# Optimization experiments

Hardware: AMD Instinct MI355X
Metric: run time of the kernel (lower is better)

The kernel has to match this reference:

```python
import jax, jax.numpy as jnp
import numpy as np

N, E, F_IN, H, C, L = 100000, 1600000, 128, 64, 16, 3
NEG_SLOPE_ATT = 0.2   # GATConv attention leaky_relu
NEG_SLOPE_ACT = 0.01  # F.leaky_relu default


def setup_inputs() -> dict:
    key = jax.random.key(0)
    ks = jax.random.split(key, 12)
    x = jax.random.normal(ks[0], (N, F_IN), dtype=jnp.float32)
    edge_index = jax.random.randint(ks[1], (2, E), 0, N, dtype=jnp.int64)
    edge_weight = jax.random.uniform(ks[2], (E,), dtype=jnp.float32)
    s = 0.05
    W_in = jax.random.normal(ks[3], (F_IN, H), dtype=jnp.float32) * s
    b_in = jnp.zeros((H,), dtype=jnp.float32)
    Wc = jax.random.normal(ks[4], (L, H, H), dtype=jnp.float32) * s
    a_src = jax.random.normal(ks[5], (L, H), dtype=jnp.float32) * s
    a_dst = jax.random.normal(ks[6], (L, H), dtype=jnp.float32) * s
    bc = jnp.zeros((L, H), dtype=jnp.float32)
    W_out = jax.random.normal(ks[7], (H, C), dtype=jnp.float32) * s
    b_out = jnp.zeros((C,), dtype=jnp.float32)
    return {"x": x, "edge_index": edge_index, "edge_weight": edge_weight,
            "W_in": W_in, "b_in": b_in, "Wc": Wc, "a_src": a_src,
            "a_dst": a_dst, "bc": bc, "W_out": W_out, "b_out": b_out}


def _gat_layer(h, src, dst, W, asrc, adst, b):
    # linear transform (no bias on lin in PyG GATConv)
    h = h @ W                                   # [N, H]
    # per-node attention contributions
    alpha_s = h @ asrc                          # [N]
    alpha_d = h @ adst                          # [N]
    e = jax.nn.leaky_relu(alpha_s[src] + alpha_d[dst], NEG_SLOPE_ATT)  # [E']
    # segment softmax over destination nodes
    m = jax.ops.segment_max(e, dst, num_segments=N)
    ex = jnp.exp(e - m[dst])
    denom = jax.ops.segment_sum(ex, dst, num_segments=N)
    w = ex / (denom[dst] + 1e-16)
    # weighted scatter-add aggregation
    out = jax.ops.segment_sum(h[src] * w[:, None], dst, num_segments=N)
    return out + b


def reference(x, edge_index, edge_weight, W_in, b_in, Wc, a_src, a_dst, bc, W_out, b_out):
    # add self-loops (PyG GATConv default)
    loops = jnp.arange(N, dtype=edge_index.dtype)
    src = jnp.concatenate([edge_index[0], loops])
    dst = jnp.concatenate([edge_index[1], loops])

    h = jax.nn.leaky_relu(x @ W_in + b_in, NEG_SLOPE_ACT)
    for l in range(L):
        h = jax.nn.leaky_relu(_gat_layer(h, src, dst, Wc[l], a_src[l], a_dst[l], bc[l]), NEG_SLOPE_ACT)
    logits = h @ W_out + b_out
    return jax.nn.log_softmax(logits, axis=-1)
```

## Files before the change

### kernel.cpp

```cpp
#include <hip/hip_runtime.h>

#define N_NODES 100000
#define E_EDGES 1600000
#define F_IN    128
#define H_DIM   64
#define C_OUT   16
#define L_LAYERS 3
#define NTOT    (E_EDGES + N_NODES)
#define MAXD    64

#define BKN2    512
#define NB2     ((N_NODES + BKN2 - 1) / BKN2)
#define BCAP    9216
#define CH      8192
#define PB      ((E_EDGES + CH - 1) / CH)

__device__ inline unsigned short f2bf(float f) {
    unsigned u = __float_as_uint(f);
    return (unsigned short)((u + 0x7FFFu + ((u >> 16) & 1u)) >> 16);
}
__device__ inline float bf_lo(unsigned p) { return __uint_as_float(p << 16); }
__device__ inline float bf_hi(unsigned p) { return __uint_as_float(p & 0xFFFF0000u); }

__global__ void detect64_kernel(const unsigned int* __restrict__ e, int* flag) {
    __shared__ int s_any;
    if (threadIdx.x == 0) s_any = 0;
    __syncthreads();
    int any = 0;
    for (int i = threadIdx.x; i < 2048; i += 256)
        if (e[2 * i + 1] != 0u) any = 1;
    if (any) atomicOr(&s_any, 1);
    __syncthreads();
    if (threadIdx.x == 0) *flag = s_any ? 0 : 1;
}

__global__ __launch_bounds__(256) void bucket_scatter2(
        const void* __restrict__ eidx, const int* __restrict__ flag,
        int* __restrict__ bcur, unsigned int* __restrict__ packed) {
    __shared__ int cnt[NB2], basel[NB2], curl[NB2], gbase[NB2];
    __shared__ int sd[256];
    __shared__ unsigned int stage[CH];
    __shared__ unsigned char bkt[CH];
    int t = threadIdx.x;
    int b0 = blockIdx.x * CH;
    int ne = min(CH, E_EDGES - b0);
    for (int i = t; i < NB2; i += 256) cnt[i] = 0;
    __syncthreads();

    int f64 = *flag;
    int es[CH / 256], ed[CH / 256];
    #pragma unroll
    for (int j = 0; j < CH / 256; ++j) {
        int idx = b0 + j * 256 + t;
        if (idx < E_EDGES) {
            if (f64) {
                es[j] = (int)((const long long*)eidx)[idx];
                ed[j] = (int)((const long long*)eidx)[E_EDGES + idx];
            } else {
                es[j] = ((const int*)eidx)[idx];
                ed[j] = ((const int*)eidx)[E_EDGES + idx];
            }
            atomicAdd(&cnt[ed[j] >> 9], 1);
        } else { es[j] = -1; }
    }
    __syncthreads();
    int v = (t < NB2) ? cnt[t] : 0;
    sd[t] = v;
    __syncthreads();
    for (int off = 1; off < 256; off <<= 1) {
        int u = (t >= off) ? sd[t - off] : 0;
        __syncthreads();
        sd[t] += u;
        __syncthreads();
    }
    if (t < NB2) {
        basel[t] = sd[t] - v;
        curl[t] = 0;
        gbase[t] = atomicAdd(&bcur[t], v);
    }
    __syncthreads();
    #pragma unroll
    for (int j = 0; j < CH / 256; ++j) {
        if (es[j] >= 0) {
            int b = ed[j] >> 9;
            int r = atomicAdd(&curl[b], 1);
            int pos = basel[b] + r;
            stage[pos] = ((unsigned)(ed[j] & (BKN2 - 1)) << 17) | (unsigned)es[j];
            bkt[pos] = (unsigned char)b;
        }
    }
    __syncthreads();
    for (int i = t; i < ne; i += 256) {
        int b = bkt[i];
        packed[(size_t)b * BCAP + gbase[b] + (i - basel[b])] = stage[i];
    }
}

__global__ __launch_bounds__(256) void bucket_scan2(
        const int* __restrict__ bcur, int* __restrict__ ebase) {
    __shared__ int sd[256];
    int t = threadIdx.x;
    int v = (t < NB2) ? bcur[t] : 0;
    sd[t] = v;
    __syncthreads();
    for (int off = 1; off < 256; off <<= 1) {
        int u = (t >= off) ? sd[t - off] : 0;
        __syncthreads();
        sd[t] += u;
        __syncthreads();
    }
    if (t < NB2) ebase[t] = sd[t] - v;
}

__global__ __launch_bounds__(256) void csr_build2(
        const unsigned int* __restrict__ packed, const int* __restrict__ bcur,
        const int* __restrict__ ebase,
        int* __restrict__ row_ptr, int* __restrict__ csr_src) {
    __shared__ int cnt[BKN2], scn[BKN2], cur[BKN2];
    int b = blockIdx.x, t = threadIdx.x;
    int nbase = b * BKN2;
    int nn = min(BKN2, N_NODES - nbase);
    int ec = bcur[b];
    size_t pbase = (size_t)b * BCAP;
    int cbase = ebase[b] + nbase;
    cnt[t] = (t < nn) ? 1 : 0;
    cnt[t + 256] = (t + 256 < nn) ? 1 : 0;
    __syncthreads();
    for (int i = t; i < ec; i += 256)
        atomicAdd(&cnt[packed[pbase + i] >> 17], 1);
    __syncthreads();
    scn[t] = cnt[t];
    scn[t + 256] = cnt[t + 256];
    __syncthreads();
    for (int off = 1; off < BKN2; off <<= 1) {
        int u0 = (t >= off) ? scn[t - off] : 0;
        int u1 = (t + 256 >= off) ? scn[t + 256 - off] : 0;
        __syncthreads();
        scn[t] += u0;
        scn[t + 256] += u1;
        __syncthreads();
    }
    #pragma unroll
    for (int q = 0; q < 2; ++q) {
        int idx = t + q * 256;
        if (idx < nn) {
            int offi = scn[idx] - cnt[idx];
            row_ptr[nbase + idx] = cbase + offi;
            csr_src[cbase + offi] = nbase + idx;
            cur[idx] = offi + 1;
        }
    }
    if (b == NB2 - 1 && t == 0) row_ptr[N_NODES] = cbase + ec + nn;
    __syncthreads();
    for (int i = t; i < ec; i += 256) {
        unsigned p = packed[pbase + i];
        int dl = p >> 17, s = (int)(p & 0x1FFFFu);
        int pos = atomicAdd(&cur[dl], 1);
        csr_src[cbase + pos] = s;
    }
}

#define GBR 64
#define KC  64
#define SAP (KC + 4)

template<int K, bool ACT, bool DOTS, bool ABF16>
__global__ __launch_bounds__(256) void gemm_lds_kernel(
        const void* __restrict__ Ain, const float* __restrict__ W,
        const float* __restrict__ bias,
        const float* __restrict__ asrc, const float* __restrict__ adst,
        unsigned* __restrict__ C, float* __restrict__ as_, float* __restrict__ ad_) {
    __shared__ __align__(16) float sW[KC * 64];
    __shared__ __align__(16) float sA[GBR][SAP];
    int t = threadIdx.x;
    int r0 = blockIdx.x * GBR;
    int wave = t >> 6, lane = t & 63;
    int tr = wave * 4 + (lane >> 4);
    int c0 = (lane & 15) * 4;

    float acc[4][4];
    #pragma unroll
    for (int i = 0; i < 4; ++i)
        #pragma unroll
        for (int j = 0; j < 4; ++j) acc[i][j] = 0.f;

    for (int kc = 0; kc < K; kc += KC) {
        if (kc) __syncthreads();
        {
            const float4* W4 = (const float4*)(W + kc * 64);
            float4* sW4 = (float4*)sW;
            for (int i = t; i < KC * 16; i += 256) sW4[i] = W4[i];
        }
        if (ABF16) {
            const unsigned* A32 = (const unsigned*)Ain;
            for (int it = 0; it < (GBR * KC / 4) / 256; ++it) {
                int idx = it * 256 + t;
                int r = idx >> 4;
                int c2 = idx & 15;
                int gr = r0 + r;
                uint2 pv = make_uint2(0u, 0u);
                if (gr < N_NODES)
                    pv = *(const uint2*)&A32[(size_t)gr * (K / 2) + kc / 2 + c2 * 2];
                sA[r][c2 * 4 + 0] = bf_lo(pv.x);
                sA[r][c2 * 4 + 1] = bf_hi(pv.x);
                sA[r][c2 * 4 + 2] = bf_lo(pv.y);
                sA[r][c2 * 4 + 3] = bf_hi(pv.y);
            }
        } else {
            const float* A = (const float*)Ain;
            for (int it = 0; it < (GBR * KC / 4) / 256; ++it) {
                int idx = it * 256 + t;
                int r = idx >> 4;
                int c4 = idx & 15;
                int gr = r0 + r;
                float4 v = make_float4(0.f, 0.f, 0.f, 0.f);
                if (gr < N_NODES) v = *(const float4*)&A[(size_t)gr * K + kc + c4 * 4];
                *(float4*)&sA[r][c4 * 4] = v;
            }
        }
        __syncthreads();
        #pragma unroll 2
        for (int kk = 0; kk < KC; kk += 4) {
            float4 w0 = *(const float4*)&sW[(kk + 0) * 64 + c0];
            float4 w1 = *(const float4*)&sW[(kk + 1) * 64 + c0];
            float4 w2 = *(const float4*)&sW[(kk + 2) * 64 + c0];
            float4 w3 = *(const float4*)&sW[(kk + 3) * 64 + c0];
            #pragma unroll
            for (int i = 0; i < 4; ++i) {
                float4 a = *(const float4*)&sA[tr + 16 * i][kk];
                acc[i][0] += a.x * w0.x + a.y * w1.x + a.z * w2.x + a.w * w3.x;
                acc[i][1] += a.x * w0.y + a.y * w1.y + a.z * w2.y + a.w * w3.y;
                acc[i][2] += a.x * w0.z + a.y * w1.z + a.z * w2.z + a.w * w3.z;
                acc[i][3] += a.x * w0.w + a.y * w1.w + a.z * w2.w + a.w * w3.w;
            }
        }
    }

    float bs[4] = {0.f, 0.f, 0.f, 0.f};
    float av[4], dv[4];
    if (ACT) {
        #pragma unroll
        for (int j = 0; j < 4; ++j) bs[j] = bias[c0 + j];
    }
    if (DOTS) {
        #pragma unroll
        for (int j = 0; j < 4; ++j) { av[j] = asrc[c0 + j]; dv[j] = adst[c0 + j]; }
    }
    #pragma unroll
    for (int i = 0; i < 4; ++i) {
        int grow = r0 + tr + 16 * i;
        if (grow >= N_NODES) continue;
        float v0 = acc[i][0], v1 = acc[i][1], v2 = acc[i][2], v3 = acc[i][3];
        if (ACT) {
            v0 += bs[0]; v0 = v0 > 0.f ? v0 : 0.01f * v0;
            v1 += bs[1]; v1 = v1 > 0.f ? v1 : 0.01f * v1;
            v2 += bs[2]; v2 = v2 > 0.f ? v2 : 0.01f * v2;
            v3 += bs[3]; v3 = v3 > 0.f ? v3 : 0.01f * v3;
        }
        unsigned p0 = (unsigned)f2bf(v0) | ((unsigned)f2bf(v1) << 16);
        unsigned p1 = (unsigned)f2bf(v2) | ((unsigned)f2bf(v3) << 16);
        *(uint2*)&C[(size_t)grow * 32 + (c0 >> 1)] = make_uint2(p0, p1);
        if (DOTS) {
            float ds = acc[i][0] * av[0] + acc[i][1] * av[1] + acc[i][2] * av[2] + acc[i][3] * av[3];
            float dd = acc[i][0] * dv[0] + acc[i][1] * dv[1] + acc[i][2] * dv[2] + acc[i][3] * dv[3];
            #pragma unroll
            for (int off = 1; off < 16; off <<= 1) {
                ds += __shfl_xor(ds, off);
                dd += __shfl_xor(dd, off);
            }
            if ((lane & 15) == 0) { as_[grow] = ds; ad_[grow] = dd; }
        }
    }
}

__global__ __launch_bounds__(256) void agg_kernel(
        const int* __restrict__ row_ptr, const int* __restrict__ csr_src,
        const float* __restrict__ as_, const float* __restrict__ ad_,
        const unsigned* __restrict__ hw32, const float* __restrict__ bc,
        unsigned* __restrict__ hout32) {
    __shared__ float exbuf[4][MAXD];
    __shared__ int   sbuf[4][MAXD];
    int wave = threadIdx.x >> 6, lane = threadIdx.x & 63;
    int node = blockIdx.x * 4 + wave;
    if (node >= N_NODES) return;
    int rs = row_ptr[node], re = row_ptr[node + 1];
    int deg = re - rs;
    float aD = ad_[node];
    float psum = 0.f;
    for (int i = lane; i < deg; i += 64) {
        int s = csr_src[rs + i];
        float v = as_[s] + aD;
        v = v > 0.f ? v : 0.2f * v;
        float p = __expf(v);
        if (deg <= MAXD) { exbuf[wave][i] = p; sbuf[wave][i] = s; }
        psum += p;
    }
    #pragma unroll
    for (int off = 32; off >= 1; off >>= 1) psum += __shfl_xor(psum, off);
    float inv = 1.f / (psum + 1e-16f);

    int half = lane >> 5, fl = lane & 31;
    float acc0 = 0.f, acc1 = 0.f;
    if (deg <= MAXD) {
        int i = half;
        for (; i + 6 < deg; i += 8) {
            unsigned o0 = ((unsigned)sbuf[wave][i]     << 5) | fl;
            unsigned o1 = ((unsigned)sbuf[wave][i + 2] << 5) | fl;
            unsigned o2 = ((unsigned)sbuf[wave][i + 4] << 5) | fl;
            unsigned o3 = ((unsigned)sbuf[wave][i + 6] << 5) | fl;
            float w0 = exbuf[wave][i]     * inv, w1 = exbuf[wave][i + 2] * inv;
            float w2 = exbuf[wave][i + 4] * inv, w3 = exbuf[wave][i + 6] * inv;
            unsigned p0 = hw32[o0];
            unsigned p1 = hw32[o1];
            unsigned p2 = hw32[o2];
            unsigned p3 = hw32[o3];
            acc0 += w0 * bf_lo(p0) + w1 * bf_lo(p1) + w2 * bf_lo(p2) + w3 * bf_lo(p3);
            acc1 += w0 * bf_hi(p0) + w1 * bf_hi(p1) + w2 * bf_hi(p2) + w3 * bf_hi(p3);
        }
        for (; i < deg; i += 2) {
            float w = exbuf[wave][i] * inv;
            unsigned p = hw32[((unsigned)sbuf[wave][i] << 5) | fl];
            acc0 += w * bf_lo(p);
            acc1 += w * bf_hi(p);
        }
    } else {
        for (int i = half; i < deg; i += 2) {
            int s = csr_src[rs + i];
            float v = as_[s] + aD;
            v = v > 0.f ? v : 0.2f * v;
            float w = __expf(v) * inv;
            unsigned p = hw32[((unsigned)s << 5) | fl];
            acc0 += w * bf_lo(p);
            acc1 += w * bf_hi(p);
        }
    }
    acc0 += __shfl_xor(acc0, 32);
    acc1 += __shfl_xor(acc1, 32);
    if (half == 0) {
        float v0 = acc0 + bc[2 * fl];
        float v1 = acc1 + bc[2 * fl + 1];
        v0 = v0 > 0.f ? v0 : 0.01f * v0;
        v1 = v1 > 0.f ? v1 : 0.01f * v1;
        hout32[((unsigned)node << 5) | fl] = (unsigned)f2bf(v0) | ((unsigned)f2bf(v1) << 16);
    }
}

__global__ __launch_bounds__(256) void out_logsoftmax_kernel(
        const unsigned* __restrict__ h32, const float* __restrict__ W,
        const float* __restrict__ b, float* __restrict__ out) {
    __shared__ float sW[H_DIM * C_OUT];
    __shared__ float sh[16][H_DIM];
    __shared__ float sb[C_OUT];
    int t = threadIdx.x;
    for (int i = t; i < H_DIM * C_OUT; i += 256) sW[i] = W[i];
    if (t < C_OUT) sb[t] = b[t];
    int row0 = blockIdx.x * 16;
    #pragma unroll
    for (int it = 0; it < 2; ++it) {
        int idx = it * 256 + t;
        int r = idx >> 5, c2 = idx & 31;
        unsigned u = h32[((unsigned)(row0 + r) << 5) | c2];
        sh[r][c2 * 2] = bf_lo(u);
        sh[r][c2 * 2 + 1] = bf_hi(u);
    }
    __syncthreads();
    int r = t >> 4, c = t & 15;
    float acc = sb[c];
    #pragma unroll
    for (int k = 0; k < H_DIM; ++k) acc += sh[r][k] * sW[k * C_OUT + c];
    float m = acc;
    #pragma unroll
    for (int off = 8; off >= 1; off >>= 1) m = fmaxf(m, __shfl_xor(m, off, 16));
    float e = __expf(acc - m);
    float ssum = e;
    #pragma unroll
    for (int off = 8; off >= 1; off >>= 1) ssum += __shfl_xor(ssum, off, 16);
    out[(row0 + r) * C_OUT + c] = acc - m - __logf(ssum);
}

extern "C" void kernel_launch(void* const* d_in, const int* in_sizes, int n_in,
                              void* d_out, int out_size, void* d_ws, size_t ws_size,
                              hipStream_t stream) {
    const float* x     = (const float*)d_in[0];
    const void*  eidx  = d_in[1];
    const float* W_in  = (const float*)d_in[3];
    const float* b_in  = (const float*)d_in[4];
    const float* Wc    = (const float*)d_in[5];
    const float* a_src = (const float*)d_in[6];
    const float* a_dst = (const float*)d_in[7];
    const float* bc    = (const float*)d_in[8];
    const float* W_out = (const float*)d_in[9];
    const float* b_out = (const float*)d_in[10];
    float* out = (float*)d_out;

    unsigned* h     = (unsigned*)d_ws;
    unsigned* hw    = h + (size_t)N_NODES * 32;
    float* as_      = (float*)(hw + (size_t)N_NODES * 32);
    float* ad_      = as_ + N_NODES;
    int*   row_ptr  = (int*)(ad_ + N_NODES);
    int*   csr_src  = row_ptr + N_NODES + 1;
    unsigned int* packed = (unsigned int*)(csr_src + NTOT);
    int*   bcur     = (int*)(packed + (size_t)NB2 * BCAP);
    int*   ebase    = bcur + NB2;
    int*   flag     = ebase + NB2;

    detect64_kernel<<<1, 256, 0, stream>>>((const unsigned int*)eidx, flag);
    hipMemsetAsync(bcur, 0, NB2 * sizeof(int), stream);
    bucket_scatter2<<<PB, 256, 0, stream>>>(eidx, flag, bcur, packed);
    bucket_scan2<<<1, 256, 0, stream>>>(bcur, ebase);
    csr_build2<<<NB2, 256, 0, stream>>>(packed, bcur, ebase, row_ptr, csr_src);

    int gblocks = (N_NODES + GBR - 1) / GBR;
    gemm_lds_kernel<F_IN, true, false, false><<<gblocks, 256, 0, stream>>>(
        x, W_in, b_in, nullptr, nullptr, h, nullptr, nullptr);

    unsigned* hin = h;
    unsigned* hx  = hw;
    for (int l = 0; l < L_LAYERS; ++l) {
        gemm_lds_kernel<H_DIM, false, true, true><<<gblocks, 256, 0, stream>>>(
            hin, Wc + l * H_DIM * H_DIM, nullptr,
            a_src + l * H_DIM, a_dst + l * H_DIM, hx, as_, ad_);
        agg_kernel<<<(N_NODES + 3) / 4, 256, 0, stream>>>(
            row_ptr, csr_src, as_, ad_, hx, bc + l * H_DIM, hin);
    }

    out_logsoftmax_kernel<<<N_NODES / 16, 256, 0, stream>>>(hin, W_out, b_out, out);
}
```

Measured before the change: 338.4 us.

## Use bf16 MFMA for per-layer GAT GEMM and defer softmax normalization

Replaces the LDS-tiled FP32 FMA GEMM for the three 64x64 layer transforms with a matrix-core kernel using mfma_f32_16x16x32_bf16 on bf16 inputs and a transposed bf16 weight copy in LDS. The attention dot products are fused into it, and results are staged through LDS so each row is written with coalesced 16-byte stores. Separately, the aggregation kernel now applies the softmax reciprocal once per output instead of per edge, and bf16 packing uses the v_cvt_pk_bf16_f32 instruction. Converting the weights to bf16 adds a little extra rounding error.

```diff
diff --git a/kernel.cpp b/kernel.cpp
--- a/kernel.cpp
+++ b/kernel.cpp
@@ -15,12 +15,20 @@
 #define CH      8192
 #define PB      ((E_EDGES + CH - 1) / CH)
 
+typedef __attribute__((ext_vector_type(8))) short short8;
+typedef __attribute__((ext_vector_type(4))) float f32x4;
+
 __device__ inline unsigned short f2bf(float f) {
     unsigned u = __float_as_uint(f);
     return (unsigned short)((u + 0x7FFFu + ((u >> 16) & 1u)) >> 16);
 }
 __device__ inline float bf_lo(unsigned p) { return __uint_as_float(p << 16); }
 __device__ inline float bf_hi(unsigned p) { return __uint_as_float(p & 0xFFFF0000u); }
+__device__ inline unsigned cvt_pk_bf16(float lo, float hi) {
+    unsigned r;
+    asm("v_cvt_pk_bf16_f32 %0, %1, %2" : "=v"(r) : "v"(lo), "v"(hi));
+    return r;
+}
 
 __global__ void detect64_kernel(const unsigned int* __restrict__ e, int* flag) {
     __shared__ int s_any;
@@ -164,12 +172,9 @@
 #define KC  64
 #define SAP (KC + 4)
 
-template<int K, bool ACT, bool DOTS, bool ABF16>
-__global__ __launch_bounds__(256) void gemm_lds_kernel(
-        const void* __restrict__ Ain, const float* __restrict__ W,
-        const float* __restrict__ bias,
-        const float* __restrict__ asrc, const float* __restrict__ adst,
-        unsigned* __restrict__ C, float* __restrict__ as_, float* __restrict__ ad_) {
+__global__ __launch_bounds__(256) void gemm_in_kernel(
+        const float* __restrict__ A, const float* __restrict__ W,
+        const float* __restrict__ bias, unsigned* __restrict__ C) {
     __shared__ __align__(16) float sW[KC * 64];
     __shared__ __align__(16) float sA[GBR][SAP];
     int t = threadIdx.x;
@@ -184,39 +189,21 @@
         #pragma unroll
         for (int j = 0; j < 4; ++j) acc[i][j] = 0.f;
 
-    for (int kc = 0; kc < K; kc += KC) {
+    for (int kc = 0; kc < F_IN; kc += KC) {
         if (kc) __syncthreads();
         {
             const float4* W4 = (const float4*)(W + kc * 64);
             float4* sW4 = (float4*)sW;
             for (int i = t; i < KC * 16; i += 256) sW4[i] = W4[i];
         }
-        if (ABF16) {
-            const unsigned* A32 = (const unsigned*)Ain;
-            for (int it = 0; it < (GBR * KC / 4) / 256; ++it) {
-                int idx = it * 256 + t;
-                int r = idx >> 4;
-                int c2 = idx & 15;
-                int gr = r0 + r;
-                uint2 pv = make_uint2(0u, 0u);
-                if (gr < N_NODES)
-                    pv = *(const uint2*)&A32[(size_t)gr * (K / 2) + kc / 2 + c2 * 2];
-                sA[r][c2 * 4 + 0] = bf_lo(pv.x);
-                sA[r][c2 * 4 + 1] = bf_hi(pv.x);
-                sA[r][c2 * 4 + 2] = bf_lo(pv.y);
-                sA[r][c2 * 4 + 3] = bf_hi(pv.y);
-            }
-        } else {
-            const float* A = (const float*)Ain;
-            for (int it = 0; it < (GBR * KC / 4) / 256; ++it) {
-                int idx = it * 256 + t;
-                int r = idx >> 4;
-                int c4 = idx & 15;
-                int gr = r0 + r;
-                float4 v = make_float4(0.f, 0.f, 0.f, 0.f);
-                if (gr < N_NODES) v = *(const float4*)&A[(size_t)gr * K + kc + c4 * 4];
-                *(float4*)&sA[r][c4 * 4] = v;
-            }
+        for (int it = 0; it < (GBR * KC / 4) / 256; ++it) {
+            int idx = it * 256 + t;
+            int r = idx >> 4;
+            int c4 = idx & 15;
+            int gr = r0 + r;
+            float4 v = make_float4(0.f, 0.f, 0.f, 0.f);
+            if (gr < N_NODES) v = *(const float4*)&A[(size_t)gr * F_IN + kc + c4 * 4];
+            *(float4*)&sA[r][c4 * 4] = v;
         }
         __syncthreads();
         #pragma unroll 2
@@ -236,40 +223,90 @@
         }
     }
 
-    float bs[4] = {0.f, 0.f, 0.f, 0.f};
-    float av[4], dv[4];
-    if (ACT) {
-        #pragma unroll
-        for (int j = 0; j < 4; ++j) bs[j] = bias[c0 + j];
-    }
-    if (DOTS) {
-        #pragma unroll
-        for (int j = 0; j < 4; ++j) { av[j] = asrc[c0 + j]; dv[j] = adst[c0 + j]; }
-    }
+    float bs[4];
+    #pragma unroll
+    for (int j = 0; j < 4; ++j) bs[j] = bias[c0 + j];
     #pragma unroll
     for (int i = 0; i < 4; ++i) {
         int grow = r0 + tr + 16 * i;
         if (grow >= N_NODES) continue;
-        float v0 = acc[i][0], v1 = acc[i][1], v2 = acc[i][2], v3 = acc[i][3];
-        if (ACT) {
-            v0 += bs[0]; v0 = v0 > 0.f ? v0 : 0.01f * v0;
-            v1 += bs[1]; v1 = v1 > 0.f ? v1 : 0.01f * v1;
-            v2 += bs[2]; v2 = v2 > 0.f ? v2 : 0.01f * v2;
-            v3 += bs[3]; v3 = v3 > 0.f ? v3 : 0.01f * v3;
-        }
-        unsigned p0 = (unsigned)f2bf(v0) | ((unsigned)f2bf(v1) << 16);
-        unsigned p1 = (unsigned)f2bf(v2) | ((unsigned)f2bf(v3) << 16);
-        *(uint2*)&C[(size_t)grow * 32 + (c0 >> 1)] = make_uint2(p0, p1);
-        if (DOTS) {
-            float ds = acc[i][0] * av[0] + acc[i][1] * av[1] + acc[i][2] * av[2] + acc[i][3] * av[3];
-            float dd = acc[i][0] * dv[0] + acc[i][1] * dv[1] + acc[i][2] * dv[2] + acc[i][3] * dv[3];
-            #pragma unroll
-            for (int off = 1; off < 16; off <<= 1) {
-                ds += __shfl_xor(ds, off);
-                dd += __shfl_xor(dd, off);
-            }
-            if ((lane & 15) == 0) { as_[grow] = ds; ad_[grow] = dd; }
-        }
+        float v0 = acc[i][0] + bs[0]; v0 = v0 > 0.f ? v0 : 0.01f * v0;
+        float v1 = acc[i][1] + bs[1]; v1 = v1 > 0.f ? v1 : 0.01f * v1;
+        float v2 = acc[i][2] + bs[2]; v2 = v2 > 0.f ? v2 : 0.01f * v2;
+        float v3 = acc[i][3] + bs[3]; v3 = v3 > 0.f ? v3 : 0.01f * v3;
+        *(uint2*)&C[(size_t)grow * 32 + (c0 >> 1)] =
+            make_uint2(cvt_pk_bf16(v0, v1), cvt_pk_bf16(v2, v3));
+    }
+}
+
+__global__ __launch_bounds__(256) void gemm_mfma_kernel(
+        const unsigned* __restrict__ A32, const float* __restrict__ W,
+        const float* __restrict__ asrc, const float* __restrict__ adst,
+        unsigned* __restrict__ C, float* __restrict__ as_, float* __restrict__ ad_) {
+    __shared__ __align__(16) unsigned short sWT[64][72];
+    __shared__ float sAv[64], sDv[64];
+    __shared__ __align__(16) float sTile[4][16 * 64];
+    int t = threadIdx.x;
+    for (int i = t; i < 64 * 64; i += 256) {
+        int k = i >> 6, j = i & 63;
+        sWT[j][k] = f2bf(W[i]);
+    }
+    if (t < 64) { sAv[t] = asrc[t]; sDv[t] = adst[t]; }
+    __syncthreads();
+
+    int wave = t >> 6, lane = t & 63;
+    int r0 = blockIdx.x * 64 + wave * 16;
+    int cj = lane & 15, kq = lane >> 4;
+
+    int ra = r0 + cj;
+    if (ra >= N_NODES) ra = N_NODES - 1;
+    const short8* arow = (const short8*)&A32[(size_t)ra * 32];
+    short8 a0 = arow[kq];
+    short8 a1 = arow[4 + kq];
+
+    f32x4 zero = {0.f, 0.f, 0.f, 0.f};
+    f32x4 acc[4] = {zero, zero, zero, zero};
+    #pragma unroll
+    for (int ct = 0; ct < 4; ++ct) {
+        short8 b0 = *(const short8*)&sWT[16 * ct + cj][kq * 8];
+        short8 b1 = *(const short8*)&sWT[16 * ct + cj][32 + kq * 8];
+        acc[ct] = __builtin_amdgcn_mfma_f32_16x16x32_bf16(a0, b0, acc[ct], 0, 0, 0);
+        acc[ct] = __builtin_amdgcn_mfma_f32_16x16x32_bf16(a1, b1, acc[ct], 0, 0, 0);
+    }
+
+    float av[4], dv[4];
+    #pragma unroll
+    for (int ct = 0; ct < 4; ++ct) { av[ct] = sAv[ct * 16 + cj]; dv[ct] = sDv[ct * 16 + cj]; }
+    #pragma unroll
+    for (int r = 0; r < 4; ++r) {
+        float ds = acc[0][r] * av[0] + acc[1][r] * av[1] + acc[2][r] * av[2] + acc[3][r] * av[3];
+        float dd = acc[0][r] * dv[0] + acc[1][r] * dv[1] + acc[2][r] * dv[2] + acc[3][r] * dv[3];
+        #pragma unroll
+        for (int off = 1; off < 16; off <<= 1) {
+            ds += __shfl_xor(ds, off);
+            dd += __shfl_xor(dd, off);
+        }
+        int grow = r0 + kq * 4 + r;
+        if (cj == 0 && grow < N_NODES) { as_[grow] = ds; ad_[grow] = dd; }
+    }
+
+    float* tl = sTile[wave];
+    #pragma unroll
+    for (int ct = 0; ct < 4; ++ct)
+        #pragma unroll
+        for (int r = 0; r < 4; ++r)
+            tl[(kq * 4 + r) * 64 + ct * 16 + cj] = acc[ct][r];
+    unsigned ur[8];
+    #pragma unroll
+    for (int i = 0; i < 8; ++i) {
+        float2 fp = *(const float2*)&tl[(lane * 8 + i) * 2];
+        ur[i] = cvt_pk_bf16(fp.x, fp.y);
+    }
+    int grow = r0 + (lane >> 2);
+    if (grow < N_NODES) {
+        uint4* dst = (uint4*)&C[(size_t)grow * 32 + (lane & 3) * 8];
+        dst[0] = make_uint4(ur[0], ur[1], ur[2], ur[3]);
+        dst[1] = make_uint4(ur[4], ur[5], ur[6], ur[7]);
     }
 }
 
@@ -308,8 +345,8 @@
             unsigned o1 = ((unsigned)sbuf[wave][i + 2] << 5) | fl;
             unsigned o2 = ((unsigned)sbuf[wave][i + 4] << 5) | fl;
             unsigned o3 = ((unsigned)sbuf[wave][i + 6] << 5) | fl;
-            float w0 = exbuf[wave][i]     * inv, w1 = exbuf[wave][i + 2] * inv;
-            float w2 = exbuf[wave][i + 4] * inv, w3 = exbuf[wave][i + 6] * inv;
+            float w0 = exbuf[wave][i],     w1 = exbuf[wave][i + 2];
+            float w2 = exbuf[wave][i + 4], w3 = exbuf[wave][i + 6];
             unsigned p0 = hw32[o0];
             unsigned p1 = hw32[o1];
             unsigned p2 = hw32[o2];
@@ -318,7 +355,7 @@
             acc1 += w0 * bf_hi(p0) + w1 * bf_hi(p1) + w2 * bf_hi(p2) + w3 * bf_hi(p3);
         }
         for (; i < deg; i += 2) {
-            float w = exbuf[wave][i] * inv;
+            float w = exbuf[wave][i];
             unsigned p = hw32[((unsigned)sbuf[wave][i] << 5) | fl];
             acc0 += w * bf_lo(p);
             acc1 += w * bf_hi(p);
@@ -328,7 +365,7 @@
             int s = csr_src[rs + i];
             float v = as_[s] + aD;
             v = v > 0.f ? v : 0.2f * v;
-            float w = __expf(v) * inv;
+            float w = __expf(v);
             unsigned p = hw32[((unsigned)s << 5) | fl];
             acc0 += w * bf_lo(p);
             acc1 += w * bf_hi(p);
@@ -337,11 +374,11 @@
     acc0 += __shfl_xor(acc0, 32);
     acc1 += __shfl_xor(acc1, 32);
     if (half == 0) {
-        float v0 = acc0 + bc[2 * fl];
-        float v1 = acc1 + bc[2 * fl + 1];
+        float v0 = acc0 * inv + bc[2 * fl];
+        float v1 = acc1 * inv + bc[2 * fl + 1];
         v0 = v0 > 0.f ? v0 : 0.01f * v0;
         v1 = v1 > 0.f ? v1 : 0.01f * v1;
-        hout32[((unsigned)node << 5) | fl] = (unsigned)f2bf(v0) | ((unsigned)f2bf(v1) << 16);
+        hout32[((unsigned)node << 5) | fl] = cvt_pk_bf16(v0, v1);
     }
 }
 
@@ -410,15 +447,14 @@
     bucket_scan2<<<1, 256, 0, stream>>>(bcur, ebase);
     csr_build2<<<NB2, 256, 0, stream>>>(packed, bcur, ebase, row_ptr, csr_src);
 
-    int gblocks = (N_NODES + GBR - 1) / GBR;
-    gemm_lds_kernel<F_IN, true, false, false><<<gblocks, 256, 0, stream>>>(
-        x, W_in, b_in, nullptr, nullptr, h, nullptr, nullptr);
+    gemm_in_kernel<<<(N_NODES + GBR - 1) / GBR, 256, 0, stream>>>(x, W_in, b_in, h);
 
     unsigned* hin = h;
     unsigned* hx  = hw;
+    int mblocks = (N_NODES + 63) / 64;
     for (int l = 0; l < L_LAYERS; ++l) {
-        gemm_lds_kernel<H_DIM, false, true, true><<<gblocks, 256, 0, stream>>>(
-            hin, Wc + l * H_DIM * H_DIM, nullptr,
+        gemm_mfma_kernel<<<mblocks, 256, 0, stream>>>(
+            hin, Wc + l * H_DIM * H_DIM,
             a_src + l * H_DIM, a_dst + l * H_DIM, hx, as_, ad_);
         agg_kernel<<<(N_NODES + 3) / 4, 256, 0, stream>>>(
             row_ptr, csr_src, as_, ad_, hx, bc + l * H_DIM, hin);
```

Result: faster. 303.8 us (-10.2%).
